# Optimization experiments

Hardware: AMD Instinct MI355X
Metric: run time of the kernel (lower is better)

The kernel has to match this reference:

```python
import jax, jax.numpy as jnp
import numpy as np

N_NODES = 262144
N_EDGES = 1048576
N_GRAPHS = 8192
F_IN = 64
UNITS = 64
N_GNN = 3
ADDUCT = 8
DENSE = 512


def setup_inputs() -> dict:
    key = jax.random.key(0)
    ks = jax.random.split(key, 16)
    x_mol = jax.random.normal(ks[0], (N_NODES, F_IN), dtype=jnp.float32)
    x_adduct = jax.random.normal(ks[1], (N_GRAPHS, ADDUCT), dtype=jnp.float32)
    edge_src = jax.random.randint(ks[2], (N_EDGES,), 0, N_NODES, dtype=jnp.int32)
    edge_dst = jax.random.randint(ks[3], (N_EDGES,), 0, N_NODES, dtype=jnp.int32)
    graph_ids = jnp.sort(jax.random.randint(ks[4], (N_NODES,), 0, N_GRAPHS, dtype=jnp.int32))
    # GCN layer params (F_IN == UNITS so all layers stack)
    gcn_W = jax.random.normal(ks[5], (N_GNN, UNITS, UNITS), dtype=jnp.float32) / np.sqrt(UNITS)
    gcn_b = jnp.zeros((N_GNN, UNITS), dtype=jnp.float32)
    # Dense head params
    d1_W = jax.random.normal(ks[6], (UNITS + ADDUCT, DENSE), dtype=jnp.float32) / np.sqrt(UNITS + ADDUCT)
    d1_b = jnp.zeros((DENSE,), dtype=jnp.float32)
    d2_W = jax.random.normal(ks[7], (DENSE, DENSE), dtype=jnp.float32) / np.sqrt(DENSE)
    d2_b = jnp.zeros((DENSE,), dtype=jnp.float32)
    out_W = jax.random.normal(ks[8], (DENSE, 1), dtype=jnp.float32) / np.sqrt(DENSE)
    out_b = jnp.zeros((1,), dtype=jnp.float32)
    return {
        'x_mol': x_mol, 'x_adduct': x_adduct,
        'edge_src': edge_src, 'edge_dst': edge_dst, 'graph_ids': graph_ids,
        'gcn_W': gcn_W, 'gcn_b': gcn_b,
        'd1_W': d1_W, 'd1_b': d1_b, 'd2_W': d2_W, 'd2_b': d2_b,
        'out_W': out_W, 'out_b': out_b,
    }


def reference(x_mol, x_adduct, edge_src, edge_dst, graph_ids,
              gcn_W, gcn_b, d1_W, d1_b, d2_W, d2_b, out_W, out_b):
    # Symmetric GCN normalization with self-loops: D^{-1/2} (A + I) D^{-1/2} X W
    deg = jax.ops.segment_sum(jnp.ones((N_EDGES,), jnp.float32), edge_dst,
                              num_segments=N_NODES) + 1.0  # [N]
    norm = jax.lax.rsqrt(deg[edge_src] * deg[edge_dst])    # [E]

    h = x_mol
    for i in range(N_GNN):
        t = h @ gcn_W[i] + gcn_b[i]                        # [N, UNITS] transform first (cheap)
        msg = t[edge_src] * norm[:, None]                  # gather over edges [E, UNITS]
        agg = jax.ops.segment_sum(msg, edge_dst, num_segments=N_NODES)
        agg = agg + t / deg[:, None]                       # self-loop term (norm = 1/deg_i)
        h = jax.nn.relu(agg)

    r = jax.ops.segment_sum(h, graph_ids, num_segments=N_GRAPHS)  # sum readout [G, UNITS]
    x = jnp.concatenate([r, x_adduct], axis=1)             # [G, UNITS+ADDUCT]
    x = jax.nn.relu(x @ d1_W + d1_b)
    x = jax.nn.relu(x @ d2_W + d2_b)
    return x @ out_W + out_b                               # [G, 1]
```

## Files before the change

### kernel.cpp

```cpp
#include <hip/hip_runtime.h>
#include <hip/hip_fp16.h>

#define NN 262144
#define NE 1048576
#define NG 8192
#define FD 64
#define AD 8
#define DN 512

__global__ void k_count(const int* __restrict__ dst, int* __restrict__ counts,
                        int* __restrict__ rank) {
  int e = blockIdx.x * 256 + threadIdx.x;
  rank[e] = atomicAdd(&counts[dst[e]], 1);
}

__global__ void k_scan1(const int* __restrict__ counts, int* __restrict__ rp,
                        int* __restrict__ bsum) {
  __shared__ int s[256];
  int tid = threadIdx.x;
  int i = blockIdx.x * 256 + tid;
  int orig = counts[i];
  s[tid] = orig;
  __syncthreads();
  for (int off = 1; off < 256; off <<= 1) {
    int v = (tid >= off) ? s[tid - off] : 0;
    __syncthreads();
    s[tid] += v;
    __syncthreads();
  }
  rp[i] = s[tid] - orig;
  if (tid == 255) bsum[blockIdx.x] = s[tid];
}

__global__ void k_scan2(int* __restrict__ bsum) {
  __shared__ int s[1024];
  int tid = threadIdx.x;
  int orig = bsum[tid];
  s[tid] = orig;
  __syncthreads();
  for (int off = 1; off < 1024; off <<= 1) {
    int v = (tid >= off) ? s[tid - off] : 0;
    __syncthreads();
    s[tid] += v;
    __syncthreads();
  }
  bsum[tid] = s[tid] - orig;
}

__global__ void k_scan3(const int* __restrict__ counts, int* __restrict__ rp,
                        const int* __restrict__ bsum, float* __restrict__ rsq) {
  int i = blockIdx.x * 256 + threadIdx.x;
  rp[i] = rp[i] + bsum[blockIdx.x];
  rsq[i] = rsqrtf((float)(counts[i] + 1));
  if (i == 0) rp[NN] = NE;
}

#define FILL_EPT 16
#define FILL_CHUNK (256 * FILL_EPT)
__global__ void k_fill(const int* __restrict__ src, const int* __restrict__ dst,
                       const int* __restrict__ rank, const int* __restrict__ rp,
                       int* __restrict__ csr_s) {
  int xcd = blockIdx.x & 7;
  int chunk = blockIdx.x >> 3;
  int base = chunk * FILL_CHUNK + threadIdx.x;
#pragma unroll
  for (int i = 0; i < FILL_EPT; i++) {
    int e = base + i * 256;
    int d = dst[e];
    if ((d >> 15) == xcd) {
      csr_s[rp[d] + rank[e]] = src[e];
    }
  }
}

__device__ __forceinline__ float4 ldrow_h(const uint2* __restrict__ th2,
                                          size_t n, int ln) {
  uint2 u = th2[n * 16 + ln];
  __half2 p0 = *reinterpret_cast<__half2*>(&u.x);
  __half2 p1 = *reinterpret_cast<__half2*>(&u.y);
  float2 f0 = __half22float2(p0);
  float2 f1 = __half22float2(p1);
  return make_float4(f0.x, f0.y, f1.x, f1.y);
}

__device__ __forceinline__ void strow_h(uint2* __restrict__ th2, size_t idx,
                                        float x, float y, float z, float w) {
  __half2 p0 = __floats2half2_rn(x, y);
  __half2 p1 = __floats2half2_rn(z, w);
  uint2 u;
  u.x = *reinterpret_cast<unsigned int*>(&p0);
  u.y = *reinterpret_cast<unsigned int*>(&p1);
  th2[idx] = u;
}

#define HS 68
__global__ void __launch_bounds__(256) k_transform(const float* __restrict__ hin,
                                                   const float* __restrict__ W,
                                                   const float* __restrict__ b,
                                                   const float* __restrict__ rsq,
                                                   uint2* __restrict__ tout) {
  __shared__ float hsT[64 * HS];
  int tid = threadIdx.x;
  size_t base = (size_t)blockIdx.x * 64 * 64;

  const float4* h4 = (const float4*)(hin + base);
#pragma unroll
  for (int j = 0; j < 4; j++) {
    int f = tid + 256 * j;
    int n = f >> 4, kq = f & 15;
    float4 v = h4[f];
    hsT[(4 * kq + 0) * HS + n] = v.x;
    hsT[(4 * kq + 1) * HS + n] = v.y;
    hsT[(4 * kq + 2) * HS + n] = v.z;
    hsT[(4 * kq + 3) * HS + n] = v.w;
  }
  __syncthreads();

  int n0 = (tid >> 4) * 4;
  int c0 = (tid & 15) * 4;
  float acc[4][4];
#pragma unroll
  for (int i = 0; i < 4; i++)
#pragma unroll
    for (int j = 0; j < 4; j++) acc[i][j] = b[c0 + j];

#pragma unroll 4
  for (int k = 0; k < 64; k++) {
    float4 av = *(const float4*)&hsT[k * HS + n0];
    float4 bv = *(const float4*)&W[k * 64 + c0];
    acc[0][0] = fmaf(av.x, bv.x, acc[0][0]);
    acc[0][1] = fmaf(av.x, bv.y, acc[0][1]);
    acc[0][2] = fmaf(av.x, bv.z, acc[0][2]);
    acc[0][3] = fmaf(av.x, bv.w, acc[0][3]);
    acc[1][0] = fmaf(av.y, bv.x, acc[1][0]);
    acc[1][1] = fmaf(av.y, bv.y, acc[1][1]);
    acc[1][2] = fmaf(av.y, bv.z, acc[1][2]);
    acc[1][3] = fmaf(av.y, bv.w, acc[1][3]);
    acc[2][0] = fmaf(av.z, bv.x, acc[2][0]);
    acc[2][1] = fmaf(av.z, bv.y, acc[2][1]);
    acc[2][2] = fmaf(av.z, bv.z, acc[2][2]);
    acc[2][3] = fmaf(av.z, bv.w, acc[2][3]);
    acc[3][0] = fmaf(av.w, bv.x, acc[3][0]);
    acc[3][1] = fmaf(av.w, bv.y, acc[3][1]);
    acc[3][2] = fmaf(av.w, bv.z, acc[3][2]);
    acc[3][3] = fmaf(av.w, bv.w, acc[3][3]);
  }

  int nbase = blockIdx.x * 64;
#pragma unroll
  for (int i = 0; i < 4; i++) {
    float rs = rsq[nbase + n0 + i];
    strow_h(tout, (size_t)(nbase + n0 + i) * 16 + (c0 >> 2),
            acc[i][0] * rs, acc[i][1] * rs, acc[i][2] * rs, acc[i][3] * rs);
  }
}

__device__ __forceinline__ void aggregate_nodes(const uint2* __restrict__ th2,
                                                const int* __restrict__ rp,
                                                const int* __restrict__ csr_s,
                                                const float* __restrict__ rsq,
                                                float* __restrict__ hacc,
                                                int nbase, int grp, int ln) {
  for (int r = 0; r < 4; r++) {
    int n = nbase + r * 16 + grp;
    int beg = rp[n], end = rp[n + 1];
    float rn = rsq[n];
    float4 a0 = ldrow_h(th2, (size_t)n, ln);
    float4 a1 = make_float4(0.f, 0.f, 0.f, 0.f);
    float4 a2 = make_float4(0.f, 0.f, 0.f, 0.f);
    float4 a3 = make_float4(0.f, 0.f, 0.f, 0.f);

    int idx = beg;
    for (; idx + 4 <= end; idx += 4) {
      int s0 = csr_s[idx + 0];
      int s1 = csr_s[idx + 1];
      int s2 = csr_s[idx + 2];
      int s3 = csr_s[idx + 3];
      float4 v0 = ldrow_h(th2, (size_t)s0, ln);
      float4 v1 = ldrow_h(th2, (size_t)s1, ln);
      float4 v2 = ldrow_h(th2, (size_t)s2, ln);
      float4 v3 = ldrow_h(th2, (size_t)s3, ln);
      a0.x += v0.x; a0.y += v0.y; a0.z += v0.z; a0.w += v0.w;
      a1.x += v1.x; a1.y += v1.y; a1.z += v1.z; a1.w += v1.w;
      a2.x += v2.x; a2.y += v2.y; a2.z += v2.z; a2.w += v2.w;
      a3.x += v3.x; a3.y += v3.y; a3.z += v3.z; a3.w += v3.w;
    }
    if (idx + 2 <= end) {
      int s0 = csr_s[idx + 0];
      int s1 = csr_s[idx + 1];
      float4 v0 = ldrow_h(th2, (size_t)s0, ln);
      float4 v1 = ldrow_h(th2, (size_t)s1, ln);
      a0.x += v0.x; a0.y += v0.y; a0.z += v0.z; a0.w += v0.w;
      a1.x += v1.x; a1.y += v1.y; a1.z += v1.z; a1.w += v1.w;
      idx += 2;
    }
    if (idx < end) {
      int s0 = csr_s[idx];
      float4 v0 = ldrow_h(th2, (size_t)s0, ln);
      a0.x += v0.x; a0.y += v0.y; a0.z += v0.z; a0.w += v0.w;
    }
    int nl = r * 16 + grp;
    float4 v;
    v.x = fmaxf(rn * ((a0.x + a1.x) + (a2.x + a3.x)), 0.f);
    v.y = fmaxf(rn * ((a0.y + a1.y) + (a2.y + a3.y)), 0.f);
    v.z = fmaxf(rn * ((a0.z + a1.z) + (a2.z + a3.z)), 0.f);
    v.w = fmaxf(rn * ((a0.w + a1.w) + (a2.w + a3.w)), 0.f);
    *(float4*)&hacc[nl * HS + 4 * ln] = v;
  }
}

__global__ void __launch_bounds__(256) k_aggT(const uint2* __restrict__ tin,
                                              const int* __restrict__ rp,
                                              const int* __restrict__ csr_s,
                                              const float* __restrict__ rsq,
                                              const float* __restrict__ W,
                                              const float* __restrict__ b,
                                              uint2* __restrict__ tout) {
  __shared__ float hacc[64 * HS];
  int tid = threadIdx.x;
  int grp = tid >> 4;
  int ln = tid & 15;
  int nbase = blockIdx.x * 64;

  aggregate_nodes(tin, rp, csr_s, rsq, hacc, nbase, grp, ln);
  __syncthreads();

  int n0 = (tid >> 4) * 4;
  int c0 = (tid & 15) * 4;
  float acc[4][4];
#pragma unroll
  for (int i = 0; i < 4; i++)
#pragma unroll
    for (int j = 0; j < 4; j++) acc[i][j] = b[c0 + j];

#pragma unroll 4
  for (int k = 0; k < 64; k++) {
    float a0 = hacc[(n0 + 0) * HS + k];
    float a1 = hacc[(n0 + 1) * HS + k];
    float a2 = hacc[(n0 + 2) * HS + k];
    float a3 = hacc[(n0 + 3) * HS + k];
    float4 bv = *(const float4*)&W[k * 64 + c0];
    acc[0][0] = fmaf(a0, bv.x, acc[0][0]);
    acc[0][1] = fmaf(a0, bv.y, acc[0][1]);
    acc[0][2] = fmaf(a0, bv.z, acc[0][2]);
    acc[0][3] = fmaf(a0, bv.w, acc[0][3]);
    acc[1][0] = fmaf(a1, bv.x, acc[1][0]);
    acc[1][1] = fmaf(a1, bv.y, acc[1][1]);
    acc[1][2] = fmaf(a1, bv.z, acc[1][2]);
    acc[1][3] = fmaf(a1, bv.w, acc[1][3]);
    acc[2][0] = fmaf(a2, bv.x, acc[2][0]);
    acc[2][1] = fmaf(a2, bv.y, acc[2][1]);
    acc[2][2] = fmaf(a2, bv.z, acc[2][2]);
    acc[2][3] = fmaf(a2, bv.w, acc[2][3]);
    acc[3][0] = fmaf(a3, bv.x, acc[3][0]);
    acc[3][1] = fmaf(a3, bv.y, acc[3][1]);
    acc[3][2] = fmaf(a3, bv.z, acc[3][2]);
    acc[3][3] = fmaf(a3, bv.w, acc[3][3]);
  }

#pragma unroll
  for (int i = 0; i < 4; i++) {
    float rs = rsq[nbase + n0 + i];
    strow_h(tout, (size_t)(nbase + n0 + i) * 16 + (c0 >> 2),
            acc[i][0] * rs, acc[i][1] * rs, acc[i][2] * rs, acc[i][3] * rs);
  }
}

__global__ void __launch_bounds__(256) k_aggR(const uint2* __restrict__ tin,
                                              const int* __restrict__ rp,
                                              const int* __restrict__ csr_s,
                                              const float* __restrict__ rsq,
                                              const int* __restrict__ gids,
                                              float* __restrict__ r) {
  __shared__ float hacc[64 * HS];
  __shared__ int gl[64];
  int tid = threadIdx.x;
  int grp = tid >> 4;
  int ln = tid & 15;
  int nbase = blockIdx.x * 64;
  if (tid < 64) gl[tid] = gids[nbase + tid];

  aggregate_nodes(tin, rp, csr_s, rsq, hacc, nbase, grp, ln);
  __syncthreads();

  int c = tid & 63;
  int row0 = (tid >> 6) * 16;
  int cur = gl[row0];
  float run = 0.f;
  for (int rr = 0; rr < 16; rr++) {
    int g = gl[row0 + rr];
    float v = hacc[(row0 + rr) * HS + c];
    if (g != cur) {
      atomicAdd(&r[(size_t)cur * 64 + c], run);
      cur = g;
      run = v;
    } else {
      run += v;
    }
  }
  atomicAdd(&r[(size_t)cur * 64 + c], run);
}

__global__ void __launch_bounds__(256) k_dense1(const float* __restrict__ r,
                                                const float* __restrict__ xa,
                                                const float* __restrict__ W1,
                                                const float* __restrict__ b1,
                                                const float* __restrict__ ob,
                                                float* __restrict__ out,
                                                float* __restrict__ y1T) {
  __shared__ float xs[8 * 72];
  int tid = threadIdx.x;
  int g0 = blockIdx.x * 8;
  if (tid < 8) out[g0 + tid] = ob[0];
  for (int i = tid; i < 8 * 72; i += 256) {
    int g = i / 72, k = i % 72;
    xs[i] = (k < 64) ? r[(size_t)(g0 + g) * 64 + k] : xa[(size_t)(g0 + g) * 8 + (k - 64)];
  }
  __syncthreads();
  float acc[8][2];
#pragma unroll
  for (int g = 0; g < 8; g++) { acc[g][0] = 0.f; acc[g][1] = 0.f; }
  for (int k = 0; k < 72; k++) {
    float w0 = W1[k * 512 + tid];
    float w1 = W1[k * 512 + 256 + tid];
#pragma unroll
    for (int g = 0; g < 8; g++) {
      float xv = xs[g * 72 + k];
      acc[g][0] = fmaf(xv, w0, acc[g][0]);
      acc[g][1] = fmaf(xv, w1, acc[g][1]);
    }
  }
  float bb0 = b1[tid], bb1 = b1[256 + tid];
  float4 v;
  v = make_float4(fmaxf(acc[0][0] + bb0, 0.f), fmaxf(acc[1][0] + bb0, 0.f),
                  fmaxf(acc[2][0] + bb0, 0.f), fmaxf(acc[3][0] + bb0, 0.f));
  *(float4*)&y1T[(size_t)tid * NG + g0] = v;
  v = make_float4(fmaxf(acc[4][0] + bb0, 0.f), fmaxf(acc[5][0] + bb0, 0.f),
                  fmaxf(acc[6][0] + bb0, 0.f), fmaxf(acc[7][0] + bb0, 0.f));
  *(float4*)&y1T[(size_t)tid * NG + g0 + 4] = v;
  v = make_float4(fmaxf(acc[0][1] + bb1, 0.f), fmaxf(acc[1][1] + bb1, 0.f),
                  fmaxf(acc[2][1] + bb1, 0.f), fmaxf(acc[3][1] + bb1, 0.f));
  *(float4*)&y1T[(size_t)(256 + tid) * NG + g0] = v;
  v = make_float4(fmaxf(acc[4][1] + bb1, 0.f), fmaxf(acc[5][1] + bb1, 0.f),
                  fmaxf(acc[6][1] + bb1, 0.f), fmaxf(acc[7][1] + bb1, 0.f));
  *(float4*)&y1T[(size_t)(256 + tid) * NG + g0 + 4] = v;
}

#define DBK 32
__global__ void __launch_bounds__(512) k_dense2(const float* __restrict__ xT,
                                                const float* __restrict__ W2,
                                                const float* __restrict__ b2,
                                                const float* __restrict__ ow,
                                                float* __restrict__ out) {
  __shared__ float xs[DBK * 128];
  __shared__ float po[128];
  int tid = threadIdx.x;
  int g0 = (blockIdx.x & 63) * 128;
  int j0 = (blockIdx.x >> 6) * 128;
  int ga = (tid & 15) * 4;
  int jb = (tid >> 4) * 4;

  int kr0 = tid >> 5, gc0 = tid & 31;
  int kr1 = (tid + 512) >> 5, gc1 = tid & 31;

  float acc[4][8];
#pragma unroll
  for (int jl = 0; jl < 4; jl++) {
    float bb = b2[j0 + jb + jl];
#pragma unroll
    for (int gg = 0; gg < 8; gg++) acc[jl][gg] = bb;
  }

  float4 r0 = ((const float4*)(xT + (size_t)kr0 * NG + g0))[gc0];
  float4 r1 = ((const float4*)(xT + (size_t)kr1 * NG + g0))[gc1];

  for (int kb = 0; kb < 512; kb += DBK) {
    __syncthreads();
    ((float4*)xs)[tid] = r0;
    ((float4*)xs)[tid + 512] = r1;
    if (kb + DBK < 512) {
      r0 = ((const float4*)(xT + (size_t)(kb + DBK + kr0) * NG + g0))[gc0];
      r1 = ((const float4*)(xT + (size_t)(kb + DBK + kr1) * NG + g0))[gc1];
    }
    __syncthreads();
#pragma unroll 4
    for (int k = 0; k < DBK; k++) {
      float4 x0 = *(const float4*)&xs[k * 128 + ga];
      float4 x1 = *(const float4*)&xs[k * 128 + 64 + ga];
      float4 w0 = *(const float4*)&W2[(size_t)(kb + k) * 512 + j0 + jb];
      float xv[8] = {x0.x, x0.y, x0.z, x0.w, x1.x, x1.y, x1.z, x1.w};
      float wv[4] = {w0.x, w0.y, w0.z, w0.w};
#pragma unroll
      for (int jj = 0; jj < 4; jj++)
#pragma unroll
        for (int gg = 0; gg < 8; gg++)
          acc[jj][gg] = fmaf(wv[jj], xv[gg], acc[jj][gg]);
    }
  }

  if (tid < 128) po[tid] = 0.f;
  __syncthreads();
  float4 owv = *(const float4*)&ow[j0 + jb];
#pragma unroll
  for (int gg = 0; gg < 8; gg++) {
    float pv = fmaxf(acc[0][gg], 0.f) * owv.x + fmaxf(acc[1][gg], 0.f) * owv.y +
               fmaxf(acc[2][gg], 0.f) * owv.z + fmaxf(acc[3][gg], 0.f) * owv.w;
    pv += __shfl_xor(pv, 16);
    pv += __shfl_xor(pv, 32);
    if ((tid & 48) == 0) {
      int gi = (gg < 4) ? (ga + gg) : (64 + ga + gg - 4);
      atomicAdd(&po[gi], pv);
    }
  }
  __syncthreads();
  if (tid < 128) atomicAdd(&out[g0 + tid], po[tid]);
}

extern "C" void kernel_launch(void* const* d_in, const int* in_sizes, int n_in,
                              void* d_out, int out_size, void* d_ws, size_t ws_size,
                              hipStream_t stream) {
  const float* x_mol    = (const float*)d_in[0];
  const float* x_adduct = (const float*)d_in[1];
  const int*   edge_src = (const int*)d_in[2];
  const int*   edge_dst = (const int*)d_in[3];
  const int*   graph_ids= (const int*)d_in[4];
  const float* gcn_W    = (const float*)d_in[5];
  const float* gcn_b    = (const float*)d_in[6];
  const float* d1W      = (const float*)d_in[7];
  const float* d1b      = (const float*)d_in[8];
  const float* d2W      = (const float*)d_in[9];
  const float* d2b      = (const float*)d_in[10];
  const float* oW       = (const float*)d_in[11];
  const float* obias    = (const float*)d_in[12];
  float* out = (float*)d_out;

  char* p = (char*)d_ws;
  auto alloc = [&](size_t bytes) {
    char* q = p;
    p += (bytes + 255) & ~(size_t)255;
    return q;
  };
  int*   counts   = (int*)alloc((size_t)NN * 4);
  int*   rp       = (int*)alloc((size_t)(NN + 1) * 4);
  int*   bsum     = (int*)alloc(1024 * 4);
  float* rsq      = (float*)alloc((size_t)NN * 4);
  int*   rank     = (int*)alloc((size_t)NE * 4);
  int*   csr_s    = (int*)alloc((size_t)NE * 4);
  uint2* th_a     = (uint2*)alloc((size_t)NN * 64 * 2);
  uint2* th_b     = (uint2*)alloc((size_t)NN * 64 * 2);
  float* r        = (float*)alloc((size_t)NG * 64 * 4);
  float* y1T      = (float*)alloc((size_t)NG * 512 * 4);

  hipMemsetAsync(counts, 0, (size_t)NN * 4, stream);
  hipMemsetAsync(r, 0, (size_t)NG * 64 * 4, stream);
  k_count<<<NE / 256, 256, 0, stream>>>(edge_dst, counts, rank);
  k_scan1<<<NN / 256, 256, 0, stream>>>(counts, rp, bsum);
  k_scan2<<<1, 1024, 0, stream>>>(bsum);
  k_scan3<<<NN / 256, 256, 0, stream>>>(counts, rp, bsum, rsq);
  k_fill<<<8 * (NE / FILL_CHUNK), 256, 0, stream>>>(edge_src, edge_dst, rank, rp, csr_s);

  k_transform<<<NN / 64, 256, 0, stream>>>(x_mol, gcn_W, gcn_b, rsq, th_a);
  k_aggT<<<NN / 64, 256, 0, stream>>>(th_a, rp, csr_s, rsq,
                                      gcn_W + (size_t)1 * 64 * 64,
                                      gcn_b + (size_t)1 * 64, th_b);
  k_aggT<<<NN / 64, 256, 0, stream>>>(th_b, rp, csr_s, rsq,
                                      gcn_W + (size_t)2 * 64 * 64,
                                      gcn_b + (size_t)2 * 64, th_a);
  k_aggR<<<NN / 64, 256, 0, stream>>>(th_a, rp, csr_s, rsq, graph_ids, r);

  k_dense1<<<NG / 8, 256, 0, stream>>>(r, x_adduct, d1W, d1b, obias, out, y1T);
  k_dense2<<<256, 512, 0, stream>>>(y1T, d2W, d2b, oW, out);
}
```

Before: 486.3 us.

## Remap dense2 threads so each wave shares uniform weight rows via scalar loads

Restructures the dense2 register tile so each wavefront owns 16 output columns and each lane owns 2 graphs. W2 reads then become wave-uniform and can be served by scalar loads, replacing per-lane vector global loads. The x tile is read as one scalar per lane from shared memory instead of float4 pairs. The final reduction drops the cross-lane shuffles and does per-lane LDS atomics instead. The trade is lower FMA-per-LDS-load reuse, and it relies on the compiler actually emitting scalar loads for the uniform weights.

```diff
diff --git a/kernel.cpp b/kernel.cpp
--- a/kernel.cpp
+++ b/kernel.cpp
@@ -357,22 +357,23 @@
   int tid = threadIdx.x;
   int g0 = (blockIdx.x & 63) * 128;
   int j0 = (blockIdx.x >> 6) * 128;
-  int ga = (tid & 15) * 4;
-  int jb = (tid >> 4) * 4;
+  int gl = tid & 63;
+  int wv = __builtin_amdgcn_readfirstlane(tid >> 6);
+  const float* Wj  = W2 + j0 + wv * 16;
+  const float* bj  = b2 + j0 + wv * 16;
+  const float* owj = ow + j0 + wv * 16;
+
+  float acc[16][2];
+#pragma unroll
+  for (int jj = 0; jj < 16; jj++) {
+    float bb = bj[jj];
+    acc[jj][0] = bb;
+    acc[jj][1] = bb;
+  }
 
   int kr0 = tid >> 5, gc0 = tid & 31;
-  int kr1 = (tid + 512) >> 5, gc1 = tid & 31;
-
-  float acc[4][8];
-#pragma unroll
-  for (int jl = 0; jl < 4; jl++) {
-    float bb = b2[j0 + jb + jl];
-#pragma unroll
-    for (int gg = 0; gg < 8; gg++) acc[jl][gg] = bb;
-  }
-
   float4 r0 = ((const float4*)(xT + (size_t)kr0 * NG + g0))[gc0];
-  float4 r1 = ((const float4*)(xT + (size_t)kr1 * NG + g0))[gc1];
+  float4 r1 = ((const float4*)(xT + (size_t)(kr0 + 16) * NG + g0))[gc0];
 
   for (int kb = 0; kb < 512; kb += DBK) {
     __syncthreads();
@@ -380,38 +381,34 @@
     ((float4*)xs)[tid + 512] = r1;
     if (kb + DBK < 512) {
       r0 = ((const float4*)(xT + (size_t)(kb + DBK + kr0) * NG + g0))[gc0];
-      r1 = ((const float4*)(xT + (size_t)(kb + DBK + kr1) * NG + g0))[gc1];
+      r1 = ((const float4*)(xT + (size_t)(kb + DBK + kr0 + 16) * NG + g0))[gc0];
     }
     __syncthreads();
 #pragma unroll 4
     for (int k = 0; k < DBK; k++) {
-      float4 x0 = *(const float4*)&xs[k * 128 + ga];
-      float4 x1 = *(const float4*)&xs[k * 128 + 64 + ga];
-      float4 w0 = *(const float4*)&W2[(size_t)(kb + k) * 512 + j0 + jb];
-      float xv[8] = {x0.x, x0.y, x0.z, x0.w, x1.x, x1.y, x1.z, x1.w};
-      float wv[4] = {w0.x, w0.y, w0.z, w0.w};
-#pragma unroll
-      for (int jj = 0; jj < 4; jj++)
-#pragma unroll
-        for (int gg = 0; gg < 8; gg++)
-          acc[jj][gg] = fmaf(wv[jj], xv[gg], acc[jj][gg]);
+      float x0 = xs[k * 128 + gl];
+      float x1 = xs[k * 128 + 64 + gl];
+      const float* wrow = Wj + (size_t)(kb + k) * 512;
+#pragma unroll
+      for (int jj = 0; jj < 16; jj++) {
+        float w = wrow[jj];
+        acc[jj][0] = fmaf(w, x0, acc[jj][0]);
+        acc[jj][1] = fmaf(w, x1, acc[jj][1]);
+      }
     }
   }
 
   if (tid < 128) po[tid] = 0.f;
   __syncthreads();
-  float4 owv = *(const float4*)&ow[j0 + jb];
-#pragma unroll
-  for (int gg = 0; gg < 8; gg++) {
-    float pv = fmaxf(acc[0][gg], 0.f) * owv.x + fmaxf(acc[1][gg], 0.f) * owv.y +
-               fmaxf(acc[2][gg], 0.f) * owv.z + fmaxf(acc[3][gg], 0.f) * owv.w;
-    pv += __shfl_xor(pv, 16);
-    pv += __shfl_xor(pv, 32);
-    if ((tid & 48) == 0) {
-      int gi = (gg < 4) ? (ga + gg) : (64 + ga + gg - 4);
-      atomicAdd(&po[gi], pv);
-    }
-  }
+  float pv0 = 0.f, pv1 = 0.f;
+#pragma unroll
+  for (int jj = 0; jj < 16; jj++) {
+    float w = owj[jj];
+    pv0 = fmaf(fmaxf(acc[jj][0], 0.f), w, pv0);
+    pv1 = fmaf(fmaxf(acc[jj][1], 0.f), w, pv1);
+  }
+  atomicAdd(&po[gl], pv0);
+  atomicAdd(&po[64 + gl], pv1);
   __syncthreads();
   if (tid < 128) atomicAdd(&out[g0 + tid], po[tid]);
 }
```

Measured after the change: 524.7 us. 7.9% more time.
